# Performance work log

Measured on AMD Instinct MI355X. Metric: run time of the kernel, lower is better.

## Reference

```python
import jax, jax.numpy as jnp
import numpy as np

B, N, P, K = 64, 64, 128, 16

def setup_inputs() -> dict:
    key = jax.random.key(0)
    k1, k2, k3, k4 = jax.random.split(key, 4)
    x = jax.random.normal(k1, (B, N, P), dtype=jnp.float32)
    idx = jax.random.randint(k2, (B, P), 0, K)
    x_mask = jax.nn.one_hot(idx, K, dtype=jnp.float32)  # [B, P, K] one-hot
    # xavier_normal_ init for weights [K, N*N]
    std = float(np.sqrt(2.0 / (K + N * N)))
    weights = std * jax.random.normal(k3, (K, N * N), dtype=jnp.float32)
    g = jax.random.uniform(k4, (N * N, N * N), dtype=jnp.float32)
    return {"x": x, "x_mask": x_mask, "weights": weights, "g": g}

def reference(x, x_mask, weights, g):
    b, n, p = x.shape
    wg = jnp.matmul(weights ** 2, g)               # [K, N*N]
    w = jnp.einsum('bpk,km->bpm', x_mask, wg)      # [B, P, N*N]
    ef = jnp.exp(-w.reshape(b, p, n, n))           # [B, P, N, N]
    # torch does x[b].reshape(p, -1, 1): row-major reinterpretation of [N,P] -> [P,N]
    xr = x.reshape(b, p, n)                        # [B, P, N]
    Z = jnp.einsum('bpij,bpj->bi', ef, xr)         # batched matvec, summed over p
    return (Z, w)
```

## Files before the change

### kernel.cpp

```cpp
#include <hip/hip_runtime.h>
#include <hip/hip_bf16.h>


typedef float f32x4 __attribute__((ext_vector_type(4)));

__device__ __forceinline__ void dma16(const void* g, void* l) {
    __builtin_amdgcn_global_load_lds(
        (const __attribute__((address_space(1))) void*)g,
        (__attribute__((address_space(3))) void*)l, 16, 0, 0);
}

__global__ __launch_bounds__(256) void k_gemm(const float* __restrict__ W,
                                              const float* __restrict__ G,
                                              float* __restrict__ part) {
    __shared__ float buf[8192];
    float4* w2t4 = (float4*)buf;
    float4* stg  = (float4*)(buf + 4096);

    const int tc  = blockIdx.x & 15;
    const int mg  = blockIdx.x >> 4;
    const int tid = threadIdx.x;
    const int wv  = tid >> 6;
    const int ln  = tid & 63;
    const int tt  = tid >> 4;
    const int t0  = tc * 256;

    {
        float v[16];
#pragma unroll
        for (int k = 0; k < 16; ++k) {
            float w = W[k * 4096 + t0 + tid];
            v[k] = w * w;
        }
#pragma unroll
        for (int q = 0; q < 4; ++q) {
            const int slot = (q + (tid >> 1)) & 3;
            w2t4[tid * 4 + slot] =
                make_float4(v[4*q], v[4*q+1], v[4*q+2], v[4*q+3]);
        }
    }

    const float4* G4 = (const float4*)G;
    const int fi  = wv * 64 + ln;
    const int tl_ = fi >> 4;
    const int mc_ = fi & 15;

    dma16(&G4[(size_t)(t0 + tl_) * 1024 + mg * 16 + mc_], &stg[wv * 64]);
    __syncthreads();

    float4 acc[16];
#pragma unroll
    for (int k = 0; k < 16; ++k) acc[k] = make_float4(0.f, 0.f, 0.f, 0.f);

    for (int s = 0; s < 16; ++s) {
        if (s < 15)
            dma16(&G4[(size_t)(t0 + (s + 1) * 16 + tl_) * 1024 + mg * 16 + mc_],
                  &stg[((s + 1) & 1) * 256 + wv * 64]);

        const float4 g4 = stg[(s & 1) * 256 + tid];
        const int r = s * 16 + tt;
#pragma unroll
        for (int q = 0; q < 4; ++q) {
            const int slot = (q + (r >> 1)) & 3;
            const float4 wq = w2t4[r * 4 + slot];
            const float* wf = (const float*)&wq;
#pragma unroll
            for (int c = 0; c < 4; ++c) {
                const float sc = wf[c];
                acc[q*4+c].x = fmaf(sc, g4.x, acc[q*4+c].x);
                acc[q*4+c].y = fmaf(sc, g4.y, acc[q*4+c].y);
                acc[q*4+c].z = fmaf(sc, g4.z, acc[q*4+c].z);
                acc[q*4+c].w = fmaf(sc, g4.w, acc[q*4+c].w);
            }
        }
        __syncthreads();
    }

    float4* red = (float4*)buf;
    float4* p4  = (float4*)part;
#pragma unroll
    for (int r = 0; r < 2; ++r) {
#pragma unroll
        for (int ks = 0; ks < 8; ++ks)
            red[ks * 256 + tid] = acc[r * 8 + ks];
        __syncthreads();
        if (tid < 128) {
            const int ks = tid >> 4;
            const int c2 = tid & 15;
            float4 s = make_float4(0.f, 0.f, 0.f, 0.f);
#pragma unroll
            for (int t2 = 0; t2 < 16; ++t2) {
                float4 v = red[ks * 256 + t2 * 16 + c2];
                s.x += v.x; s.y += v.y; s.z += v.z; s.w += v.w;
            }
            const int k = r * 8 + ks;
            p4[(size_t)tc * 16384 + (size_t)k * 1024 + mg * 16 + c2] = s;
        }
        __syncthreads();
    }
}

__global__ __launch_bounds__(64) void k_reduce(const float* __restrict__ part,
                                               float* __restrict__ wg,
                                               float* __restrict__ E) {
    const int q = blockIdx.x * 64 + threadIdx.x;
    const float4* p4 = (const float4*)part;
    float4 s = make_float4(0.f, 0.f, 0.f, 0.f);
#pragma unroll
    for (int tc = 0; tc < 16; ++tc) {
        float4 v = p4[(size_t)tc * 16384 + q];
        s.x += v.x; s.y += v.y; s.z += v.z; s.w += v.w;
    }
    ((float4*)wg)[q] = s;
    ((float4*)E)[q] = make_float4(expf(-s.x), expf(-s.y), expf(-s.z), expf(-s.w));
}

__global__ __launch_bounds__(256) void k_wz(const float* __restrict__ x,
                                            const float* __restrict__ xmask,
                                            const float* __restrict__ wg,
                                            const float* __restrict__ E,
                                            float* __restrict__ wout,
                                            float* __restrict__ zout) {
    __shared__ float sw[4][16][64];
    __shared__ int   idx[128];
    __shared__ float zr[16][16];
    const int tid = threadIdx.x;

    if (blockIdx.x < 8192) {
        const int bp = blockIdx.x;
        const float* xm = xmask + (size_t)bp * 16;
        int k = 0;
#pragma unroll
        for (int i = 0; i < 16; ++i) k = (xm[i] > 0.5f) ? i : k;
        const f32x4* src = (const f32x4*)(wg + (size_t)k * 4096);
        f32x4*       dst = (f32x4*)(wout + (size_t)bp * 4096);
#pragma unroll
        for (int c = 0; c < 4; ++c) {
            f32x4 v = src[c * 256 + tid];
            __builtin_nontemporal_store(v, &dst[c * 256 + tid]);
        }
        return;
    }

    const int zb = blockIdx.x - 8192;
    const int b  = zb >> 2;
    const int iq = zb & 3;
    const int wv = tid >> 6;
    const int ln = tid & 63;

    if (tid < 128) {
        const float* xm = xmask + ((size_t)b * 128 + tid) * 16;
        int k = 0;
#pragma unroll
        for (int i = 0; i < 16; ++i) k = (xm[i] > 0.5f) ? i : k;
        idx[tid] = k;
    }
#pragma unroll
    for (int c = 0; c < 16; ++c)
        ((float*)sw)[c * 256 + tid] = 0.f;
    __syncthreads();

    const float* xb = x + (size_t)b * 8192;
    for (int p = wv * 32; p < wv * 32 + 32; ++p) {
        int k = idx[p];
        sw[wv][k][ln] += xb[p * 64 + ln];
    }
    __syncthreads();

    for (int e = tid; e < 1024; e += 256) {
        int k2 = e >> 6, j = e & 63;
        sw[0][k2][j] = sw[0][k2][j] + sw[1][k2][j] + sw[2][k2][j] + sw[3][k2][j];
    }
    __syncthreads();

    {
        const int k  = tid >> 4;
        const int il = tid & 15;
        const int i  = iq * 16 + il;
        float a = 0.f;
        const float4* Er = (const float4*)(E + (size_t)k * 4096 + i * 64);
        const float4* sr = (const float4*)(&sw[0][k][0]);
#pragma unroll
        for (int j4 = 0; j4 < 16; ++j4) {
            float4 e4 = Er[j4];
            float4 s4 = sr[j4];
            a = fmaf(e4.x, s4.x, a);
            a = fmaf(e4.y, s4.y, a);
            a = fmaf(e4.z, s4.z, a);
            a = fmaf(e4.w, s4.w, a);
        }
        zr[k][il] = a;
    }
    __syncthreads();
    if (tid < 16) {
        float s = 0.f;
#pragma unroll
        for (int k = 0; k < 16; ++k) s += zr[k][tid];
        zout[b * 64 + iq * 16 + tid] = s;
    }
}

extern "C" void kernel_launch(void* const* d_in, const int* in_sizes, int n_in,
                              void* d_out, int out_size, void* d_ws, size_t ws_size,
                              hipStream_t stream) {
    const float* x     = (const float*)d_in[0];
    const float* xmask = (const float*)d_in[1];
    const float* W     = (const float*)d_in[2];
    const float* G     = (const float*)d_in[3];

    float* zout = (float*)d_out;
    float* wout = (float*)d_out + 4096;

    float* wg = (float*)d_ws;
    float* E  = wg + 65536;

    float* part = wout;

    k_gemm  <<<1024, 256, 0, stream>>>(W, G, part);
    k_reduce<<<256,  64,  0, stream>>>(part, wg, E);
    k_wz    <<<8448, 256, 0, stream>>>(x, xmask, wg, E, wout, zout);
}
```

Measured before the change: 51.51 us.

## Bucket rows by mask class and broadcast wg slices from registers

Adds extra blocks to the GEMM kernel. One block buckets the (b,p) rows by their one-hot class into a rows/counts table, and the others precompute the per-batch masked x sums into a workspace buffer. The output-writing kernel then has 512 blocks that each load one wg slice once into registers and stream it to every row of that class. This replaces 8192 blocks that each re-decoded the mask and re-read wg. The fixed 768-slot capacity per class assumes a roughly uniform class distribution. With far fewer blocks doing long serial store loops, the write kernel may have less memory-level parallelism.

```diff
diff --git a/kernel.cpp b/kernel.cpp
--- a/kernel.cpp
+++ b/kernel.cpp
@@ -12,16 +12,63 @@
 
 __global__ __launch_bounds__(256) void k_gemm(const float* __restrict__ W,
                                               const float* __restrict__ G,
-                                              float* __restrict__ part) {
+                                              float* __restrict__ part,
+                                              const float* __restrict__ x,
+                                              const float* __restrict__ xmask,
+                                              float* __restrict__ sbuf,
+                                              int* __restrict__ counts,
+                                              int* __restrict__ rows) {
     __shared__ float buf[8192];
-    float4* w2t4 = (float4*)buf;
-    float4* stg  = (float4*)(buf + 4096);
-
-    const int tc  = blockIdx.x & 15;
-    const int mg  = blockIdx.x >> 4;
     const int tid = threadIdx.x;
     const int wv  = tid >> 6;
     const int ln  = tid & 63;
+
+    if (blockIdx.x >= 1088) {
+        int* cnt16 = (int*)buf;
+        if (tid < 16) cnt16[tid] = 0;
+        __syncthreads();
+        for (int i = 0; i < 32; ++i) {
+            const int bp = tid * 32 + i;
+            const float* xm = xmask + (size_t)bp * 16;
+            int k = 0;
+#pragma unroll
+            for (int j = 0; j < 16; ++j) k = (xm[j] > 0.5f) ? j : k;
+            const int pos = atomicAdd(&cnt16[k], 1);
+            rows[k * 768 + pos] = bp;
+        }
+        __syncthreads();
+        if (tid < 16) counts[tid] = cnt16[tid];
+        return;
+    }
+
+    if (blockIdx.x >= 1024) {
+        const int b = blockIdx.x - 1024;
+        float* sw  = buf;
+        int*  idxp = (int*)(buf + 4096);
+        if (tid < 128) {
+            const float* xm = xmask + ((size_t)b * 128 + tid) * 16;
+            int k = 0;
+#pragma unroll
+            for (int i = 0; i < 16; ++i) k = (xm[i] > 0.5f) ? i : k;
+            idxp[tid] = k;
+        }
+#pragma unroll
+        for (int c = 0; c < 16; ++c) sw[c * 256 + tid] = 0.f;
+        __syncthreads();
+        const float* xb = x + (size_t)b * 8192;
+        for (int p = wv * 32; p < wv * 32 + 32; ++p)
+            sw[wv * 1024 + idxp[p] * 64 + ln] += xb[p * 64 + ln];
+        __syncthreads();
+        for (int e = tid; e < 1024; e += 256)
+            sbuf[b * 1024 + e] = sw[e] + sw[1024 + e] + sw[2048 + e] + sw[3072 + e];
+        return;
+    }
+
+    float4* w2t4 = (float4*)buf;
+    float4* stg  = (float4*)(buf + 4096);
+
+    const int tc  = blockIdx.x & 15;
+    const int mg  = blockIdx.x >> 4;
     const int tt  = tid >> 4;
     const int t0  = tc * 256;
 
@@ -115,71 +162,47 @@
     ((float4*)E)[q] = make_float4(expf(-s.x), expf(-s.y), expf(-s.z), expf(-s.w));
 }
 
-__global__ __launch_bounds__(256) void k_wz(const float* __restrict__ x,
-                                            const float* __restrict__ xmask,
+__global__ __launch_bounds__(256) void k_sz(const int* __restrict__ counts,
+                                            const int* __restrict__ rows,
                                             const float* __restrict__ wg,
                                             const float* __restrict__ E,
+                                            const float* __restrict__ sbuf,
                                             float* __restrict__ wout,
                                             float* __restrict__ zout) {
-    __shared__ float sw[4][16][64];
-    __shared__ int   idx[128];
+    __shared__ int   lrows[128];
     __shared__ float zr[16][16];
     const int tid = threadIdx.x;
 
-    if (blockIdx.x < 8192) {
-        const int bp = blockIdx.x;
-        const float* xm = xmask + (size_t)bp * 16;
-        int k = 0;
-#pragma unroll
-        for (int i = 0; i < 16; ++i) k = (xm[i] > 0.5f) ? i : k;
-        const f32x4* src = (const f32x4*)(wg + (size_t)k * 4096);
-        f32x4*       dst = (f32x4*)(wout + (size_t)bp * 4096);
-#pragma unroll
-        for (int c = 0; c < 4; ++c) {
-            f32x4 v = src[c * 256 + tid];
-            __builtin_nontemporal_store(v, &dst[c * 256 + tid]);
+    if (blockIdx.x < 512) {
+        const int k  = blockIdx.x >> 5;
+        const int ms = (blockIdx.x >> 3) & 3;
+        const int rh = blockIdx.x & 7;
+        const f32x4 v = *(const f32x4*)(wg + (size_t)k * 4096 + ms * 1024 + tid * 4);
+        const int cnt   = counts[k];
+        const int chunk = (cnt + 7) >> 3;
+        const int r0 = rh * chunk;
+        const int r1 = (r0 + chunk < cnt) ? (r0 + chunk) : cnt;
+        const int n  = r1 - r0;
+        if (tid < n) lrows[tid] = rows[k * 768 + r0 + tid];
+        __syncthreads();
+        for (int i = 0; i < n; ++i) {
+            const int row = lrows[i];
+            __builtin_nontemporal_store(
+                v, (f32x4*)(wout + (size_t)row * 4096 + ms * 1024 + tid * 4));
         }
         return;
     }
 
-    const int zb = blockIdx.x - 8192;
+    const int zb = blockIdx.x - 512;
     const int b  = zb >> 2;
     const int iq = zb & 3;
-    const int wv = tid >> 6;
-    const int ln = tid & 63;
-
-    if (tid < 128) {
-        const float* xm = xmask + ((size_t)b * 128 + tid) * 16;
-        int k = 0;
-#pragma unroll
-        for (int i = 0; i < 16; ++i) k = (xm[i] > 0.5f) ? i : k;
-        idx[tid] = k;
-    }
-#pragma unroll
-    for (int c = 0; c < 16; ++c)
-        ((float*)sw)[c * 256 + tid] = 0.f;
-    __syncthreads();
-
-    const float* xb = x + (size_t)b * 8192;
-    for (int p = wv * 32; p < wv * 32 + 32; ++p) {
-        int k = idx[p];
-        sw[wv][k][ln] += xb[p * 64 + ln];
-    }
-    __syncthreads();
-
-    for (int e = tid; e < 1024; e += 256) {
-        int k2 = e >> 6, j = e & 63;
-        sw[0][k2][j] = sw[0][k2][j] + sw[1][k2][j] + sw[2][k2][j] + sw[3][k2][j];
-    }
-    __syncthreads();
-
     {
         const int k  = tid >> 4;
         const int il = tid & 15;
         const int i  = iq * 16 + il;
         float a = 0.f;
         const float4* Er = (const float4*)(E + (size_t)k * 4096 + i * 64);
-        const float4* sr = (const float4*)(&sw[0][k][0]);
+        const float4* sr = (const float4*)(sbuf + (size_t)b * 1024 + k * 64);
 #pragma unroll
         for (int j4 = 0; j4 < 16; ++j4) {
             float4 e4 = Er[j4];
@@ -195,7 +218,7 @@
     if (tid < 16) {
         float s = 0.f;
 #pragma unroll
-        for (int k = 0; k < 16; ++k) s += zr[k][tid];
+        for (int kk = 0; kk < 16; ++kk) s += zr[kk][tid];
         zout[b * 64 + iq * 16 + tid] = s;
     }
 }
@@ -211,12 +234,15 @@
     float* zout = (float*)d_out;
     float* wout = (float*)d_out + 4096;
 
-    float* wg = (float*)d_ws;
-    float* E  = wg + 65536;
+    float* wg     = (float*)d_ws;
+    float* E      = wg + 65536;
+    float* sbuf   = E + 65536;
+    int*   counts = (int*)(sbuf + 65536);
+    int*   rows   = counts + 16;
 
     float* part = wout;
 
-    k_gemm  <<<1024, 256, 0, stream>>>(W, G, part);
+    k_gemm  <<<1089, 256, 0, stream>>>(W, G, part, x, xmask, sbuf, counts, rows);
     k_reduce<<<256,  64,  0, stream>>>(part, wg, E);
-    k_wz    <<<8448, 256, 0, stream>>>(x, xmask, wg, E, wout, zout);
-}
+    k_sz    <<<768,  256, 0, stream>>>(counts, rows, wg, E, sbuf, wout, zout);
+}
```

After: 67.77 us. 31.6% more time.

## Stage wg slices in LDS and stream w rows from persistent per-batch blocks

Applied to the files above, without the earlier changes.

Changes the w-output scatter from one block per (b,p) row to 256 blocks. Each block caches a quarter-column slice of all 16 wg rows in LDS (64KB) and writes 128 rows of output from it. The aim is to cut block launch overhead and repeated global reads of wg, and to make the streaming stores denser. In exchange the grid shrinks from 8448 to 512 blocks, and the large LDS footprint limits occupancy, so the write bandwidth of 128MB-scale output may be harder to saturate.

```diff
diff --git a/kernel.cpp b/kernel.cpp
--- a/kernel.cpp
+++ b/kernel.cpp
@@ -115,38 +115,64 @@
     ((float4*)E)[q] = make_float4(expf(-s.x), expf(-s.y), expf(-s.z), expf(-s.w));
 }
 
-__global__ __launch_bounds__(256) void k_wz(const float* __restrict__ x,
+__global__ __launch_bounds__(256) void k_sz(const float* __restrict__ x,
                                             const float* __restrict__ xmask,
                                             const float* __restrict__ wg,
                                             const float* __restrict__ E,
                                             float* __restrict__ wout,
                                             float* __restrict__ zout) {
-    __shared__ float sw[4][16][64];
-    __shared__ int   idx[128];
-    __shared__ float zr[16][16];
+    __shared__ float lds[16512];
     const int tid = threadIdx.x;
 
-    if (blockIdx.x < 8192) {
-        const int bp = blockIdx.x;
-        const float* xm = xmask + (size_t)bp * 16;
-        int k = 0;
-#pragma unroll
-        for (int i = 0; i < 16; ++i) k = (xm[i] > 0.5f) ? i : k;
-        const f32x4* src = (const f32x4*)(wg + (size_t)k * 4096);
-        f32x4*       dst = (f32x4*)(wout + (size_t)bp * 4096);
-#pragma unroll
-        for (int c = 0; c < 4; ++c) {
-            f32x4 v = src[c * 256 + tid];
-            __builtin_nontemporal_store(v, &dst[c * 256 + tid]);
+    if (blockIdx.x < 256) {
+        const int b  = blockIdx.x >> 2;
+        const int ms = blockIdx.x & 3;
+        float4* wgs4 = (float4*)lds;
+        int*    idxl = (int*)(lds + 16384);
+
+        if (tid < 128) {
+            const float* xm = xmask + ((size_t)b * 128 + tid) * 16;
+            int k = 0;
+#pragma unroll
+            for (int j = 0; j < 16; ++j) k = (xm[j] > 0.5f) ? j : k;
+            idxl[tid] = k;
+        }
+        const float4* wg4 = (const float4*)wg;
+#pragma unroll
+        for (int c = 0; c < 16; ++c) {
+            const int e   = c * 256 + tid;
+            const int k   = e >> 8;
+            const int off = e & 255;
+            wgs4[e] = wg4[(size_t)k * 1024 + ms * 256 + off];
+        }
+        __syncthreads();
+
+        float* wb = wout + (size_t)b * 128 * 4096 + (size_t)ms * 1024;
+        for (int p = 0; p < 128; p += 4) {
+            const int k0 = idxl[p + 0];
+            const int k1 = idxl[p + 1];
+            const int k2 = idxl[p + 2];
+            const int k3 = idxl[p + 3];
+            f32x4 v0 = ((f32x4*)lds)[k0 * 256 + tid];
+            f32x4 v1 = ((f32x4*)lds)[k1 * 256 + tid];
+            f32x4 v2 = ((f32x4*)lds)[k2 * 256 + tid];
+            f32x4 v3 = ((f32x4*)lds)[k3 * 256 + tid];
+            __builtin_nontemporal_store(v0, (f32x4*)(wb + (size_t)(p + 0) * 4096) + tid);
+            __builtin_nontemporal_store(v1, (f32x4*)(wb + (size_t)(p + 1) * 4096) + tid);
+            __builtin_nontemporal_store(v2, (f32x4*)(wb + (size_t)(p + 2) * 4096) + tid);
+            __builtin_nontemporal_store(v3, (f32x4*)(wb + (size_t)(p + 3) * 4096) + tid);
         }
         return;
     }
 
-    const int zb = blockIdx.x - 8192;
+    const int zb = blockIdx.x - 256;
     const int b  = zb >> 2;
     const int iq = zb & 3;
     const int wv = tid >> 6;
     const int ln = tid & 63;
+    float* sw  = lds;
+    int*   idx = (int*)(lds + 4096);
+    float* zr  = lds + 4224;
 
     if (tid < 128) {
         const float* xm = xmask + ((size_t)b * 128 + tid) * 16;
@@ -157,20 +183,18 @@
     }
 #pragma unroll
     for (int c = 0; c < 16; ++c)
-        ((float*)sw)[c * 256 + tid] = 0.f;
+        sw[c * 256 + tid] = 0.f;
     __syncthreads();
 
     const float* xb = x + (size_t)b * 8192;
     for (int p = wv * 32; p < wv * 32 + 32; ++p) {
         int k = idx[p];
-        sw[wv][k][ln] += xb[p * 64 + ln];
-    }
-    __syncthreads();
-
-    for (int e = tid; e < 1024; e += 256) {
-        int k2 = e >> 6, j = e & 63;
-        sw[0][k2][j] = sw[0][k2][j] + sw[1][k2][j] + sw[2][k2][j] + sw[3][k2][j];
-    }
+        sw[wv * 1024 + k * 64 + ln] += xb[p * 64 + ln];
+    }
+    __syncthreads();
+
+    for (int e = tid; e < 1024; e += 256)
+        sw[e] = sw[e] + sw[1024 + e] + sw[2048 + e] + sw[3072 + e];
     __syncthreads();
 
     {
@@ -179,7 +203,7 @@
         const int i  = iq * 16 + il;
         float a = 0.f;
         const float4* Er = (const float4*)(E + (size_t)k * 4096 + i * 64);
-        const float4* sr = (const float4*)(&sw[0][k][0]);
+        const float4* sr = (const float4*)(sw + k * 64);
 #pragma unroll
         for (int j4 = 0; j4 < 16; ++j4) {
             float4 e4 = Er[j4];
@@ -189,13 +213,13 @@
             a = fmaf(e4.z, s4.z, a);
             a = fmaf(e4.w, s4.w, a);
         }
-        zr[k][il] = a;
+        zr[k * 16 + il] = a;
     }
     __syncthreads();
     if (tid < 16) {
         float s = 0.f;
 #pragma unroll
-        for (int k = 0; k < 16; ++k) s += zr[k][tid];
+        for (int k = 0; k < 16; ++k) s += zr[k * 16 + tid];
         zout[b * 64 + iq * 16 + tid] = s;
     }
 }
@@ -218,5 +242,5 @@
 
     k_gemm  <<<1024, 256, 0, stream>>>(W, G, part);
     k_reduce<<<256,  64,  0, stream>>>(part, wg, E);
-    k_wz    <<<8448, 256, 0, stream>>>(x, xmask, wg, E, wout, zout);
-}
+    k_sz    <<<512,  256, 0, stream>>>(x, xmask, wg, E, wout, zout);
+}
```

Result: slower. 64.32 us (+24.9%).
